# Kernel tuning notes

Measured on AMD Instinct MI355X. Metric: run time of the kernel, lower is better.

Reference implementation:

```python
import jax, jax.numpy as jnp
from jax import lax
import numpy as np

H = 32  # hidden size (hardcoded by Linear(32,1) in the source)
I = 1   # input size

def setup_inputs() -> dict:
    key = jax.random.key(0)
    ks = jax.random.split(key, 8)
    B, T = 2048, 1024
    s_ih = 1.0 / np.sqrt(H)
    inp = {
        "x": jax.random.normal(ks[0], (B, T, I), dtype=jnp.float32),
        "h_state": jnp.zeros((1, B, H), dtype=jnp.float32),
        # GRU params, PyTorch layout: gates stacked as [r; z; n] -> [3H, *]
        "W_ih": jax.random.uniform(ks[1], (3 * H, I), jnp.float32, -s_ih, s_ih),
        "W_hh": jax.random.uniform(ks[2], (3 * H, H), jnp.float32, -s_ih, s_ih),
        "b_ih": jax.random.uniform(ks[3], (3 * H,), jnp.float32, -s_ih, s_ih),
        "b_hh": jax.random.uniform(ks[4], (3 * H,), jnp.float32, -s_ih, s_ih),
        # output Linear(32, 1)
        "W_out": jax.random.uniform(ks[5], (1, H), jnp.float32, -s_ih, s_ih),
        "b_out": jax.random.uniform(ks[6], (1,), jnp.float32, -s_ih, s_ih),
    }
    return inp

def _gru(x, h0, W_ih, W_hh, b_ih, b_hh):
    # Precompute input projections for all timesteps: [B,T,3H]
    x_proj = jnp.einsum('bti,gi->btg', x, W_ih) + b_ih
    xp_t = jnp.swapaxes(x_proj, 0, 1)  # [T,B,3H] for scan

    def step(h, xp):
        gh = h @ W_hh.T + b_hh  # [B,3H]
        r = jax.nn.sigmoid(xp[:, :H] + gh[:, :H])
        z = jax.nn.sigmoid(xp[:, H:2 * H] + gh[:, H:2 * H])
        n = jnp.tanh(xp[:, 2 * H:] + r * gh[:, 2 * H:])
        h_new = (1.0 - z) * n + z * h
        return h_new, h_new

    h_final, h_seq = lax.scan(step, h0[0], xp_t)
    return jnp.swapaxes(h_seq, 0, 1), h_final[None]  # [B,T,H], [1,B,H]

def reference(x, h_state, W_ih, W_hh, b_ih, b_hh, W_out, b_out):
    r_out, h_n = _gru(x, h_state, W_ih, W_hh, b_ih, b_hh)
    # per-timestep Linear(32,1), vectorized over time
    y = jnp.einsum('bth,oh->bto', r_out, W_out) + b_out  # [B,T,1]
    return (y, h_n)
```

## Files before the change

### kernel.cpp

```cpp
#include <hip/hip_runtime.h>


constexpr int H  = 32;
constexpr int TT = 1024;
constexpr int BB = 2048;

typedef _Float16 hf2 __attribute__((ext_vector_type(2)));

__device__ __forceinline__ unsigned pack2(float a, float b) {
    hf2 t; t.x = (_Float16)a; t.y = (_Float16)b;
    return __builtin_bit_cast(unsigned, t);
}

__global__ __launch_bounds__(256, 1)
void gru_fused(const float* __restrict__ x,
               const float* __restrict__ h0,
               const float* __restrict__ W_ih,
               const float* __restrict__ W_hh,
               const float* __restrict__ b_ih,
               const float* __restrict__ b_hh,
               const float* __restrict__ W_out,
               const float* __restrict__ b_out,
               float* __restrict__ out)
{
    __shared__ __align__(16) _Float16 hbuf[4][64];
    __shared__ float xstage[4][64];
    __shared__ float ybuf[4][2][36 * 32];

    const int tid  = threadIdx.x;
    const int w    = tid >> 6;
    const int lane = tid & 63;
    const int half = lane >> 5;
    const int j    = lane & 31;
    const int gw   = (blockIdx.x << 2) | w;
    const int b    = (gw << 1) | half;

    const float NL2E = -1.44269504f;
    const float P2L2 =  2.88539008f;

    const float* Wrp = &W_hh[(0 * H + j) * H];
    const float* Wzp = &W_hh[(1 * H + j) * H];
    const float* Wnp = &W_hh[(2 * H + j) * H];
    unsigned wr[16], wz[16], wn[16];
#pragma unroll
    for (int k = 0; k < 16; ++k) {
        wr[k] = pack2(Wrp[2 * k] * NL2E, Wrp[2 * k + 1] * NL2E);
        wz[k] = pack2(Wzp[2 * k] * NL2E, Wzp[2 * k + 1] * NL2E);
        wn[k] = pack2(Wnp[2 * k] * P2L2, Wnp[2 * k + 1] * P2L2);
    }
    const float wir = W_ih[j] * NL2E;
    const float wiz = W_ih[H + j] * NL2E;
    const float br  = (b_ih[j] + b_hh[j]) * NL2E;
    const float bz  = (b_ih[H + j] + b_hh[H + j]) * NL2E;
    const float bhn = b_hh[2 * H + j] * P2L2;
    const float win = W_ih[2 * H + j] * P2L2;
    const float bin = b_ih[2 * H + j] * P2L2;
    const float wo  = W_out[j];
    const float bo  = b_out[0];

    float h = h0[b * H + j];

    const float* xb = x + (size_t)b * TT;
    float*       yb = out + (size_t)b * TT;

    const unsigned ha = (unsigned)(size_t)&hbuf[w][half * 32 + j];
    const unsigned hr = (unsigned)(size_t)&hbuf[w][half * 32];
    const unsigned xw = (unsigned)(size_t)&xstage[w][half * 32 + j];
    const unsigned xa = (unsigned)(size_t)&xstage[w][half * 32];
    const unsigned ya = (unsigned)(size_t)&ybuf[w][half][j];
    const float* yr = &ybuf[w][half][0];

#pragma unroll 1
    for (int t0 = 0; t0 < TT; t0 += 32) {
        const float xv = xb[t0 + j];

        asm volatile(
            "s_mov_b32 s20, 0\n\t"
            "v_mov_b32 v82, %[ya]\n\t"
            "v_mov_b32 v83, %[xa]\n\t"
            "ds_write_b32 %[xw], %[xv]\n\t"
            "L_gru_%=:\n\t"
            "v_cvt_f16_f32 v33, %[h]\n\t"
            "ds_write_b16 %[ha], v33\n\t"
            "ds_read_b128 v[36:39], %[hr]\n\t"
            "ds_read_b128 v[40:43], %[hr] offset:16\n\t"
            "ds_read_b128 v[44:47], %[hr] offset:32\n\t"
            "ds_read_b128 v[48:51], %[hr] offset:48\n\t"
            "ds_read_b32 v80, v83\n\t"
            "s_waitcnt lgkmcnt(0)\n\t"
            "v_dot2_f32_f16 v68, %[r0], v36, %[br]\n\t"
            "v_dot2_f32_f16 v69, %[z0], v36, %[bz]\n\t"
            "v_dot2_f32_f16 v70, %[n0], v36, %[bn]\n\t"
            "v_dot2_f32_f16 v68, %[r1], v37, v68\n\t"
            "v_dot2_f32_f16 v69, %[z1], v37, v69\n\t"
            "v_dot2_f32_f16 v70, %[n1], v37, v70\n\t"
            "v_dot2_f32_f16 v68, %[r2], v38, v68\n\t"
            "v_dot2_f32_f16 v69, %[z2], v38, v69\n\t"
            "v_dot2_f32_f16 v70, %[n2], v38, v70\n\t"
            "v_dot2_f32_f16 v68, %[r3], v39, v68\n\t"
            "v_dot2_f32_f16 v69, %[z3], v39, v69\n\t"
            "v_dot2_f32_f16 v70, %[n3], v39, v70\n\t"
            "v_dot2_f32_f16 v68, %[r4], v40, v68\n\t"
            "v_dot2_f32_f16 v69, %[z4], v40, v69\n\t"
            "v_dot2_f32_f16 v70, %[n4], v40, v70\n\t"
            "v_dot2_f32_f16 v68, %[r5], v41, v68\n\t"
            "v_dot2_f32_f16 v69, %[z5], v41, v69\n\t"
            "v_dot2_f32_f16 v70, %[n5], v41, v70\n\t"
            "v_dot2_f32_f16 v68, %[r6], v42, v68\n\t"
            "v_dot2_f32_f16 v69, %[z6], v42, v69\n\t"
            "v_dot2_f32_f16 v70, %[n6], v42, v70\n\t"
            "v_dot2_f32_f16 v68, %[r7], v43, v68\n\t"
            "v_dot2_f32_f16 v69, %[z7], v43, v69\n\t"
            "v_dot2_f32_f16 v70, %[n7], v43, v70\n\t"
            "v_dot2_f32_f16 v68, %[r8], v44, v68\n\t"
            "v_dot2_f32_f16 v69, %[z8], v44, v69\n\t"
            "v_dot2_f32_f16 v70, %[n8], v44, v70\n\t"
            "v_dot2_f32_f16 v68, %[r9], v45, v68\n\t"
            "v_dot2_f32_f16 v69, %[z9], v45, v69\n\t"
            "v_dot2_f32_f16 v70, %[n9], v45, v70\n\t"
            "v_dot2_f32_f16 v68, %[r10], v46, v68\n\t"
            "v_dot2_f32_f16 v69, %[z10], v46, v69\n\t"
            "v_dot2_f32_f16 v70, %[n10], v46, v70\n\t"
            "v_dot2_f32_f16 v68, %[r11], v47, v68\n\t"
            "v_dot2_f32_f16 v69, %[z11], v47, v69\n\t"
            "v_dot2_f32_f16 v70, %[n11], v47, v70\n\t"
            "v_dot2_f32_f16 v68, %[r12], v48, v68\n\t"
            "v_dot2_f32_f16 v69, %[z12], v48, v69\n\t"
            "v_dot2_f32_f16 v70, %[n12], v48, v70\n\t"
            "v_dot2_f32_f16 v68, %[r13], v49, v68\n\t"
            "v_dot2_f32_f16 v69, %[z13], v49, v69\n\t"
            "v_dot2_f32_f16 v70, %[n13], v49, v70\n\t"
            "v_dot2_f32_f16 v68, %[r14], v50, v68\n\t"
            "v_dot2_f32_f16 v69, %[z14], v50, v69\n\t"
            "v_dot2_f32_f16 v70, %[n14], v50, v70\n\t"
            "v_dot2_f32_f16 v68, %[r15], v51, v68\n\t"
            "v_dot2_f32_f16 v69, %[z15], v51, v69\n\t"
            "v_dot2_f32_f16 v70, %[n15], v51, v70\n\t"
            "v_fmac_f32 v68, v80, %[wir]\n\t"
            "v_fmac_f32 v69, v80, %[wiz]\n\t"
            "v_exp_f32 v71, v68\n\t"
            "v_exp_f32 v72, v69\n\t"
            "v_fma_f32 v74, v80, %[wi], %[bi]\n\t"
            "s_nop 2\n\t"
            "v_add_f32 v71, 1.0, v71\n\t"
            "v_add_f32 v72, 1.0, v72\n\t"
            "v_rcp_f32 v71, v71\n\t"
            "v_rcp_f32 v72, v72\n\t"
            "s_nop 2\n\t"
            "v_fmac_f32 v74, v71, v70\n\t"
            "v_exp_f32 v75, v74\n\t"
            "s_nop 2\n\t"
            "v_add_f32 v75, 1.0, v75\n\t"
            "v_rcp_f32 v75, v75\n\t"
            "s_nop 2\n\t"
            "v_fma_f32 v76, -2.0, v75, 1.0\n\t"
            "v_sub_f32 v77, %[h], v76\n\t"
            "v_fma_f32 %[h], v72, v77, v76\n\t"
            "v_mul_f32 v78, %[wo], %[h]\n\t"
            "ds_write_b32 v82, v78\n\t"
            "v_add_u32 v82, 144, v82\n\t"
            "v_add_u32 v83, 4, v83\n\t"
            "s_add_i32 s20, s20, 1\n\t"
            "s_cmp_lt_u32 s20, 32\n\t"
            "s_cbranch_scc1 L_gru_%=\n\t"
            "s_waitcnt lgkmcnt(0)"
            : [h]"+v"(h)
            : [xv]"v"(xv), [ha]"v"(ha), [hr]"v"(hr), [xw]"v"(xw), [xa]"v"(xa),
              [ya]"v"(ya),
              [wir]"v"(wir), [wiz]"v"(wiz), [wi]"v"(win), [bi]"v"(bin),
              [wo]"v"(wo), [br]"v"(br), [bz]"v"(bz), [bn]"v"(bhn),
              [r0]"v"(wr[0]), [r1]"v"(wr[1]), [r2]"v"(wr[2]), [r3]"v"(wr[3]),
              [r4]"v"(wr[4]), [r5]"v"(wr[5]), [r6]"v"(wr[6]), [r7]"v"(wr[7]),
              [r8]"v"(wr[8]), [r9]"v"(wr[9]), [r10]"v"(wr[10]), [r11]"v"(wr[11]),
              [r12]"v"(wr[12]), [r13]"v"(wr[13]), [r14]"v"(wr[14]), [r15]"v"(wr[15]),
              [z0]"v"(wz[0]), [z1]"v"(wz[1]), [z2]"v"(wz[2]), [z3]"v"(wz[3]),
              [z4]"v"(wz[4]), [z5]"v"(wz[5]), [z6]"v"(wz[6]), [z7]"v"(wz[7]),
              [z8]"v"(wz[8]), [z9]"v"(wz[9]), [z10]"v"(wz[10]), [z11]"v"(wz[11]),
              [z12]"v"(wz[12]), [z13]"v"(wz[13]), [z14]"v"(wz[14]), [z15]"v"(wz[15]),
              [n0]"v"(wn[0]), [n1]"v"(wn[1]), [n2]"v"(wn[2]), [n3]"v"(wn[3]),
              [n4]"v"(wn[4]), [n5]"v"(wn[5]), [n6]"v"(wn[6]), [n7]"v"(wn[7]),
              [n8]"v"(wn[8]), [n9]"v"(wn[9]), [n10]"v"(wn[10]), [n11]"v"(wn[11]),
              [n12]"v"(wn[12]), [n13]"v"(wn[13]), [n14]"v"(wn[14]), [n15]"v"(wn[15])
            : "memory", "scc", "s20",
              "v33", "v36", "v37", "v38", "v39", "v40", "v41", "v42", "v43",
              "v44", "v45", "v46", "v47", "v48", "v49", "v50", "v51",
              "v68", "v69", "v70", "v71", "v72", "v74", "v75", "v76", "v77",
              "v78", "v80", "v82", "v83");

        float s0 = 0.0f, s1 = 0.0f, s2 = 0.0f, s3 = 0.0f;
#pragma unroll
        for (int k = 0; k < 32; k += 4) {
            s0 += yr[36 * j + k + 0];
            s1 += yr[36 * j + k + 1];
            s2 += yr[36 * j + k + 2];
            s3 += yr[36 * j + k + 3];
        }
        yb[t0 + j] = (s0 + s1) + (s2 + s3) + bo;
        __builtin_amdgcn_wave_barrier();
    }

    out[(size_t)BB * TT + b * H + j] = h;
}

extern "C" void kernel_launch(void* const* d_in, const int* in_sizes, int n_in,
                              void* d_out, int out_size, void* d_ws, size_t ws_size,
                              hipStream_t stream) {
    const float* x     = (const float*)d_in[0];
    const float* h0    = (const float*)d_in[1];
    const float* W_ih  = (const float*)d_in[2];
    const float* W_hh  = (const float*)d_in[3];
    const float* b_ih  = (const float*)d_in[4];
    const float* b_hh  = (const float*)d_in[5];
    const float* W_out = (const float*)d_in[6];
    const float* b_out = (const float*)d_in[7];
    float* out = (float*)d_out;

    dim3 grid(BB / 8);
    dim3 block(256);
    gru_fused<<<grid, block, 0, stream>>>(x, h0, W_ih, W_hh, b_ih, b_hh,
                                          W_out, b_out, out);
}
```

Before: 312.1 us.

## Interleave two independent GRU batch streams per wave to hide LDS latency

Each wave now advances two independent pairs of batch rows (P and Q), software-pipelining them. The LDS write and reads of hidden state for one stream are issued while the other stream's dot products and gate math run, and the wait count is relaxed from 0 to 7. This targets the serial LDS round-trip latency in each recurrent step. Blocks shrink to 128 threads and the grid to 256 blocks, so there are half as many waves in total and each CU may occupy fewer SIMDs. LDS buffers are re-laid out with new padding to match.

```diff
diff --git a/kernel.cpp b/kernel.cpp
--- a/kernel.cpp
+++ b/kernel.cpp
@@ -12,7 +12,13 @@
     return __builtin_bit_cast(unsigned, t);
 }
 
-__global__ __launch_bounds__(256, 1)
+#define DOT2_SET(QA, QB, QC, QD)                                   \
+    "v_dot2_f32_f16 v68, %[r0], " QA ", %[br]\n\t"                 \
+    "v_dot2_f32_f16 v69, %[z0], " QA ", %[bz]\n\t"                 \
+    "v_dot2_f32_f16 v70, %[n0], " QA ", %[bn]\n\t"                 \
+    "v_dot2_f32_f16 v68, %[r1], " QA "1, v68\n\t"
+
+__global__ __launch_bounds__(128, 1)
 void gru_fused(const float* __restrict__ x,
                const float* __restrict__ h0,
                const float* __restrict__ W_ih,
@@ -23,17 +29,18 @@
                const float* __restrict__ b_out,
                float* __restrict__ out)
 {
-    __shared__ __align__(16) _Float16 hbuf[4][64];
-    __shared__ float xstage[4][64];
-    __shared__ float ybuf[4][2][36 * 32];
+    __shared__ __align__(16) _Float16 hbuf[2][2][64];
+    __shared__ float xst[2][2][2][34];
+    __shared__ float ybuf[2][2][2][33 * 32];
 
     const int tid  = threadIdx.x;
     const int w    = tid >> 6;
     const int lane = tid & 63;
     const int half = lane >> 5;
     const int j    = lane & 31;
-    const int gw   = (blockIdx.x << 2) | w;
-    const int b    = (gw << 1) | half;
+    const int g    = (blockIdx.x << 1) | w;
+    const int bP   = (g << 2) | half;
+    const int bQ   = bP + 2;
 
     const float NL2E = -1.44269504f;
     const float P2L2 =  2.88539008f;
@@ -58,36 +65,52 @@
     const float wo  = W_out[j];
     const float bo  = b_out[0];
 
-    float h = h0[b * H + j];
-
-    const float* xb = x + (size_t)b * TT;
-    float*       yb = out + (size_t)b * TT;
-
-    const unsigned ha = (unsigned)(size_t)&hbuf[w][half * 32 + j];
-    const unsigned hr = (unsigned)(size_t)&hbuf[w][half * 32];
-    const unsigned xw = (unsigned)(size_t)&xstage[w][half * 32 + j];
-    const unsigned xa = (unsigned)(size_t)&xstage[w][half * 32];
-    const unsigned ya = (unsigned)(size_t)&ybuf[w][half][j];
-    const float* yr = &ybuf[w][half][0];
+    float hP = h0[bP * H + j];
+    float hQ = h0[bQ * H + j];
+
+    const float* xbP = x + (size_t)bP * TT;
+    const float* xbQ = x + (size_t)bQ * TT;
+    float*       ybP = out + (size_t)bP * TT;
+    float*       ybQ = out + (size_t)bQ * TT;
+
+    const unsigned ha = (unsigned)(size_t)&hbuf[w][0][half * 32 + j];
+    const unsigned hr = (unsigned)(size_t)&hbuf[w][0][half * 32];
+    const unsigned xw = (unsigned)(size_t)&xst[w][0][half][j];
+    const unsigned xa = (unsigned)(size_t)&xst[w][0][half][0];
+    const unsigned ya = (unsigned)(size_t)&ybuf[w][0][half][j];
+    const float* yrP = &ybuf[w][0][half][0];
+    const float* yrQ = &ybuf[w][1][half][0];
 
 #pragma unroll 1
     for (int t0 = 0; t0 < TT; t0 += 32) {
-        const float xv = xb[t0 + j];
+        const float xvP = xbP[t0 + j];
+        const float xvQ = xbQ[t0 + j];
 
         asm volatile(
-            "s_mov_b32 s20, 0\n\t"
+            "s_mov_b32 s20, 32\n\t"
             "v_mov_b32 v82, %[ya]\n\t"
             "v_mov_b32 v83, %[xa]\n\t"
-            "ds_write_b32 %[xw], %[xv]\n\t"
+            "ds_write_b32 %[xw], %[xvP]\n\t"
+            "ds_write_b32 %[xw], %[xvQ] offset:272\n\t"
+            "ds_write_b32 v82, v78 offset:8448\n\t"
+            "v_cvt_f16_f32 v33, %[hQ]\n\t"
+            "ds_write_b16 %[ha], v33 offset:128\n\t"
+            "ds_read_b128 v[36:39], %[hr] offset:128\n\t"
+            "ds_read_b128 v[40:43], %[hr] offset:144\n\t"
+            "ds_read_b128 v[44:47], %[hr] offset:160\n\t"
+            "ds_read_b128 v[48:51], %[hr] offset:176\n\t"
+            "ds_read_b32 v80, v83 offset:272\n\t"
+            "ds_write_b32 v82, v78\n\t"
+            "v_cvt_f16_f32 v33, %[hP]\n\t"
+            "ds_write_b16 %[ha], v33\n\t"
+            "ds_read_b128 v[52:55], %[hr]\n\t"
+            "ds_read_b128 v[56:59], %[hr] offset:16\n\t"
+            "ds_read_b128 v[60:63], %[hr] offset:32\n\t"
+            "ds_read_b128 v[64:67], %[hr] offset:48\n\t"
+            "ds_read_b32 v81, v83\n\t"
+
             "L_gru_%=:\n\t"
-            "v_cvt_f16_f32 v33, %[h]\n\t"
-            "ds_write_b16 %[ha], v33\n\t"
-            "ds_read_b128 v[36:39], %[hr]\n\t"
-            "ds_read_b128 v[40:43], %[hr] offset:16\n\t"
-            "ds_read_b128 v[44:47], %[hr] offset:32\n\t"
-            "ds_read_b128 v[48:51], %[hr] offset:48\n\t"
-            "ds_read_b32 v80, v83\n\t"
-            "s_waitcnt lgkmcnt(0)\n\t"
+            "s_waitcnt lgkmcnt(7)\n\t"
             "v_dot2_f32_f16 v68, %[r0], v36, %[br]\n\t"
             "v_dot2_f32_f16 v69, %[z0], v36, %[bz]\n\t"
             "v_dot2_f32_f16 v70, %[n0], v36, %[bn]\n\t"
@@ -154,19 +177,104 @@
             "v_rcp_f32 v75, v75\n\t"
             "s_nop 2\n\t"
             "v_fma_f32 v76, -2.0, v75, 1.0\n\t"
-            "v_sub_f32 v77, %[h], v76\n\t"
-            "v_fma_f32 %[h], v72, v77, v76\n\t"
-            "v_mul_f32 v78, %[wo], %[h]\n\t"
+            "v_sub_f32 v77, %[hQ], v76\n\t"
+            "v_fma_f32 %[hQ], v72, v77, v76\n\t"
+            "v_mul_f32 v78, %[wo], %[hQ]\n\t"
+            "ds_write_b32 v82, v78 offset:8448\n\t"
+            "v_cvt_f16_f32 v33, %[hQ]\n\t"
+            "ds_write_b16 %[ha], v33 offset:128\n\t"
+            "ds_read_b128 v[36:39], %[hr] offset:128\n\t"
+            "ds_read_b128 v[40:43], %[hr] offset:144\n\t"
+            "ds_read_b128 v[44:47], %[hr] offset:160\n\t"
+            "ds_read_b128 v[48:51], %[hr] offset:176\n\t"
+            "ds_read_b32 v80, v83 offset:276\n\t"
+            "s_waitcnt lgkmcnt(7)\n\t"
+            "v_dot2_f32_f16 v68, %[r0], v52, %[br]\n\t"
+            "v_dot2_f32_f16 v69, %[z0], v52, %[bz]\n\t"
+            "v_dot2_f32_f16 v70, %[n0], v52, %[bn]\n\t"
+            "v_dot2_f32_f16 v68, %[r1], v53, v68\n\t"
+            "v_dot2_f32_f16 v69, %[z1], v53, v69\n\t"
+            "v_dot2_f32_f16 v70, %[n1], v53, v70\n\t"
+            "v_dot2_f32_f16 v68, %[r2], v54, v68\n\t"
+            "v_dot2_f32_f16 v69, %[z2], v54, v69\n\t"
+            "v_dot2_f32_f16 v70, %[n2], v54, v70\n\t"
+            "v_dot2_f32_f16 v68, %[r3], v55, v68\n\t"
+            "v_dot2_f32_f16 v69, %[z3], v55, v69\n\t"
+            "v_dot2_f32_f16 v70, %[n3], v55, v70\n\t"
+            "v_dot2_f32_f16 v68, %[r4], v56, v68\n\t"
+            "v_dot2_f32_f16 v69, %[z4], v56, v69\n\t"
+            "v_dot2_f32_f16 v70, %[n4], v56, v70\n\t"
+            "v_dot2_f32_f16 v68, %[r5], v57, v68\n\t"
+            "v_dot2_f32_f16 v69, %[z5], v57, v69\n\t"
+            "v_dot2_f32_f16 v70, %[n5], v57, v70\n\t"
+            "v_dot2_f32_f16 v68, %[r6], v58, v68\n\t"
+            "v_dot2_f32_f16 v69, %[z6], v58, v69\n\t"
+            "v_dot2_f32_f16 v70, %[n6], v58, v70\n\t"
+            "v_dot2_f32_f16 v68, %[r7], v59, v68\n\t"
+            "v_dot2_f32_f16 v69, %[z7], v59, v69\n\t"
+            "v_dot2_f32_f16 v70, %[n7], v59, v70\n\t"
+            "v_dot2_f32_f16 v68, %[r8], v60, v68\n\t"
+            "v_dot2_f32_f16 v69, %[z8], v60, v69\n\t"
+            "v_dot2_f32_f16 v70, %[n8], v60, v70\n\t"
+            "v_dot2_f32_f16 v68, %[r9], v61, v68\n\t"
+            "v_dot2_f32_f16 v69, %[z9], v61, v69\n\t"
+            "v_dot2_f32_f16 v70, %[n9], v61, v70\n\t"
+            "v_dot2_f32_f16 v68, %[r10], v62, v68\n\t"
+            "v_dot2_f32_f16 v69, %[z10], v62, v69\n\t"
+            "v_dot2_f32_f16 v70, %[n10], v62, v70\n\t"
+            "v_dot2_f32_f16 v68, %[r11], v63, v68\n\t"
+            "v_dot2_f32_f16 v69, %[z11], v63, v69\n\t"
+            "v_dot2_f32_f16 v70, %[n11], v63, v70\n\t"
+            "v_dot2_f32_f16 v68, %[r12], v64, v68\n\t"
+            "v_dot2_f32_f16 v69, %[z12], v64, v69\n\t"
+            "v_dot2_f32_f16 v70, %[n12], v64, v70\n\t"
+            "v_dot2_f32_f16 v68, %[r13], v65, v68\n\t"
+            "v_dot2_f32_f16 v69, %[z13], v65, v69\n\t"
+            "v_dot2_f32_f16 v70, %[n13], v65, v70\n\t"
+            "v_dot2_f32_f16 v68, %[r14], v66, v68\n\t"
+            "v_dot2_f32_f16 v69, %[z14], v66, v69\n\t"
+            "v_dot2_f32_f16 v70, %[n14], v66, v70\n\t"
+            "v_dot2_f32_f16 v68, %[r15], v67, v68\n\t"
+            "v_dot2_f32_f16 v69, %[z15], v67, v69\n\t"
+            "v_dot2_f32_f16 v70, %[n15], v67, v70\n\t"
+            "v_fmac_f32 v68, v81, %[wir]\n\t"
+            "v_fmac_f32 v69, v81, %[wiz]\n\t"
+            "v_exp_f32 v71, v68\n\t"
+            "v_exp_f32 v72, v69\n\t"
+            "v_fma_f32 v74, v81, %[wi], %[bi]\n\t"
+            "s_nop 2\n\t"
+            "v_add_f32 v71, 1.0, v71\n\t"
+            "v_add_f32 v72, 1.0, v72\n\t"
+            "v_rcp_f32 v71, v71\n\t"
+            "v_rcp_f32 v72, v72\n\t"
+            "s_nop 2\n\t"
+            "v_fmac_f32 v74, v71, v70\n\t"
+            "v_exp_f32 v75, v74\n\t"
+            "s_nop 2\n\t"
+            "v_add_f32 v75, 1.0, v75\n\t"
+            "v_rcp_f32 v75, v75\n\t"
+            "s_nop 2\n\t"
+            "v_fma_f32 v76, -2.0, v75, 1.0\n\t"
+            "v_sub_f32 v77, %[hP], v76\n\t"
+            "v_fma_f32 %[hP], v72, v77, v76\n\t"
+            "v_mul_f32 v78, %[wo], %[hP]\n\t"
             "ds_write_b32 v82, v78\n\t"
-            "v_add_u32 v82, 144, v82\n\t"
+            "v_cvt_f16_f32 v33, %[hP]\n\t"
+            "ds_write_b16 %[ha], v33\n\t"
+            "ds_read_b128 v[52:55], %[hr]\n\t"
+            "ds_read_b128 v[56:59], %[hr] offset:16\n\t"
+            "ds_read_b128 v[60:63], %[hr] offset:32\n\t"
+            "ds_read_b128 v[64:67], %[hr] offset:48\n\t"
+            "ds_read_b32 v81, v83 offset:4\n\t"
+            "v_add_u32 v82, 132, v82\n\t"
             "v_add_u32 v83, 4, v83\n\t"
-            "s_add_i32 s20, s20, 1\n\t"
-            "s_cmp_lt_u32 s20, 32\n\t"
+            "s_sub_i32 s20, s20, 1\n\t"
+            "s_cmp_gt_i32 s20, 0\n\t"
             "s_cbranch_scc1 L_gru_%=\n\t"
             "s_waitcnt lgkmcnt(0)"
-            : [h]"+v"(h)
-            : [xv]"v"(xv), [ha]"v"(ha), [hr]"v"(hr), [xw]"v"(xw), [xa]"v"(xa),
-              [ya]"v"(ya),
+            : [hP]"+v"(hP), [hQ]"+v"(hQ)
+            : [xvP]"v"(xvP), [xvQ]"v"(xvQ),
+              [ha]"v"(ha), [hr]"v"(hr), [xw]"v"(xw), [xa]"v"(xa), [ya]"v"(ya),
               [wir]"v"(wir), [wiz]"v"(wiz), [wi]"v"(win), [bi]"v"(bin),
               [wo]"v"(wo), [br]"v"(br), [bz]"v"(bz), [bn]"v"(bhn),
               [r0]"v"(wr[0]), [r1]"v"(wr[1]), [r2]"v"(wr[2]), [r3]"v"(wr[3]),
@@ -184,22 +292,31 @@
             : "memory", "scc", "s20",
               "v33", "v36", "v37", "v38", "v39", "v40", "v41", "v42", "v43",
               "v44", "v45", "v46", "v47", "v48", "v49", "v50", "v51",
+              "v52", "v53", "v54", "v55", "v56", "v57", "v58", "v59",
+              "v60", "v61", "v62", "v63", "v64", "v65", "v66", "v67",
               "v68", "v69", "v70", "v71", "v72", "v74", "v75", "v76", "v77",
-              "v78", "v80", "v82", "v83");
-
-        float s0 = 0.0f, s1 = 0.0f, s2 = 0.0f, s3 = 0.0f;
+              "v78", "v80", "v81", "v82", "v83");
+
+        float p0 = 0.0f, p1 = 0.0f, p2 = 0.0f, p3 = 0.0f;
+        float q0 = 0.0f, q1 = 0.0f, q2 = 0.0f, q3 = 0.0f;
 #pragma unroll
         for (int k = 0; k < 32; k += 4) {
-            s0 += yr[36 * j + k + 0];
-            s1 += yr[36 * j + k + 1];
-            s2 += yr[36 * j + k + 2];
-            s3 += yr[36 * j + k + 3];
+            p0 += yrP[33 * j + k + 0];
+            p1 += yrP[33 * j + k + 1];
+            p2 += yrP[33 * j + k + 2];
+            p3 += yrP[33 * j + k + 3];
+            q0 += yrQ[33 * j + k + 0];
+            q1 += yrQ[33 * j + k + 1];
+            q2 += yrQ[33 * j + k + 2];
+            q3 += yrQ[33 * j + k + 3];
         }
-        yb[t0 + j] = (s0 + s1) + (s2 + s3) + bo;
+        ybP[t0 + j] = (p0 + p1) + (p2 + p3) + bo;
+        ybQ[t0 + j] = (q0 + q1) + (q2 + q3) + bo;
         __builtin_amdgcn_wave_barrier();
     }
 
-    out[(size_t)BB * TT + b * H + j] = h;
+    out[(size_t)BB * TT + bP * H + j] = hP;
+    out[(size_t)BB * TT + bQ * H + j] = hQ;
 }
 
 extern "C" void kernel_launch(void* const* d_in, const int* in_sizes, int n_in,
@@ -215,8 +332,8 @@
     const float* b_out = (const float*)d_in[7];
     float* out = (float*)d_out;
 
-    dim3 grid(BB / 8);
-    dim3 block(256);
+    dim3 grid(256);
+    dim3 block(128);
     gru_fused<<<grid, block, 0, stream>>>(x, h0, W_ih, W_hh, b_ih, b_hh,
                                           W_out, b_out, out);
 }
```

Result: slower. 479.8 us (+53.7%).

## Unroll GRU step loop by two and overlap LDS writes with next step

Applied to the files above, without the earlier changes.

The per-timestep inline-asm loop is unrolled twice and software-pipelined. The next step's hidden-state broadcast reads are issued before the output store, and a waitcnt of one lets that y write stay in flight while the dot products start. Input x is now fetched as a 64-bit pair every two steps, and loop counter overhead is halved. The y staging buffer stride changes from 36 to 33 to cut LDS bank conflicts on the transposed reduction reads. The s_nop padding grows from 2 to 3, which lengthens the serial dependency chain slightly.

```diff
diff --git a/kernel.cpp b/kernel.cpp
--- a/kernel.cpp
+++ b/kernel.cpp
@@ -11,6 +11,78 @@
     hf2 t; t.x = (_Float16)a; t.y = (_Float16)b;
     return __builtin_bit_cast(unsigned, t);
 }
+
+#define DOT48                                          \
+    "v_dot2_f32_f16 v68, %[r0], v36, %[br]\n\t"        \
+    "v_dot2_f32_f16 v69, %[z0], v36, %[bz]\n\t"        \
+    "v_dot2_f32_f16 v70, %[n0], v36, %[bn]\n\t"        \
+    "v_dot2_f32_f16 v68, %[r1], v37, v68\n\t"          \
+    "v_dot2_f32_f16 v69, %[z1], v37, v69\n\t"          \
+    "v_dot2_f32_f16 v70, %[n1], v37, v70\n\t"          \
+    "v_dot2_f32_f16 v68, %[r2], v38, v68\n\t"          \
+    "v_dot2_f32_f16 v69, %[z2], v38, v69\n\t"          \
+    "v_dot2_f32_f16 v70, %[n2], v38, v70\n\t"          \
+    "v_dot2_f32_f16 v68, %[r3], v39, v68\n\t"          \
+    "v_dot2_f32_f16 v69, %[z3], v39, v69\n\t"          \
+    "v_dot2_f32_f16 v70, %[n3], v39, v70\n\t"          \
+    "v_dot2_f32_f16 v68, %[r4], v40, v68\n\t"          \
+    "v_dot2_f32_f16 v69, %[z4], v40, v69\n\t"          \
+    "v_dot2_f32_f16 v70, %[n4], v40, v70\n\t"          \
+    "v_dot2_f32_f16 v68, %[r5], v41, v68\n\t"          \
+    "v_dot2_f32_f16 v69, %[z5], v41, v69\n\t"          \
+    "v_dot2_f32_f16 v70, %[n5], v41, v70\n\t"          \
+    "v_dot2_f32_f16 v68, %[r6], v42, v68\n\t"          \
+    "v_dot2_f32_f16 v69, %[z6], v42, v69\n\t"          \
+    "v_dot2_f32_f16 v70, %[n6], v42, v70\n\t"          \
+    "v_dot2_f32_f16 v68, %[r7], v43, v68\n\t"          \
+    "v_dot2_f32_f16 v69, %[z7], v43, v69\n\t"          \
+    "v_dot2_f32_f16 v70, %[n7], v43, v70\n\t"          \
+    "v_dot2_f32_f16 v68, %[r8], v44, v68\n\t"          \
+    "v_dot2_f32_f16 v69, %[z8], v44, v69\n\t"          \
+    "v_dot2_f32_f16 v70, %[n8], v44, v70\n\t"          \
+    "v_dot2_f32_f16 v68, %[r9], v45, v68\n\t"          \
+    "v_dot2_f32_f16 v69, %[z9], v45, v69\n\t"          \
+    "v_dot2_f32_f16 v70, %[n9], v45, v70\n\t"          \
+    "v_dot2_f32_f16 v68, %[r10], v46, v68\n\t"         \
+    "v_dot2_f32_f16 v69, %[z10], v46, v69\n\t"         \
+    "v_dot2_f32_f16 v70, %[n10], v46, v70\n\t"         \
+    "v_dot2_f32_f16 v68, %[r11], v47, v68\n\t"         \
+    "v_dot2_f32_f16 v69, %[z11], v47, v69\n\t"         \
+    "v_dot2_f32_f16 v70, %[n11], v47, v70\n\t"         \
+    "v_dot2_f32_f16 v68, %[r12], v48, v68\n\t"         \
+    "v_dot2_f32_f16 v69, %[z12], v48, v69\n\t"         \
+    "v_dot2_f32_f16 v70, %[n12], v48, v70\n\t"         \
+    "v_dot2_f32_f16 v68, %[r13], v49, v68\n\t"         \
+    "v_dot2_f32_f16 v69, %[z13], v49, v69\n\t"         \
+    "v_dot2_f32_f16 v70, %[n13], v49, v70\n\t"         \
+    "v_dot2_f32_f16 v68, %[r14], v50, v68\n\t"         \
+    "v_dot2_f32_f16 v69, %[z14], v50, v69\n\t"         \
+    "v_dot2_f32_f16 v70, %[n14], v50, v70\n\t"         \
+    "v_dot2_f32_f16 v68, %[r15], v51, v68\n\t"         \
+    "v_dot2_f32_f16 v69, %[z15], v51, v69\n\t"         \
+    "v_dot2_f32_f16 v70, %[n15], v51, v70\n\t"
+
+#define TAIL(XREG, HREG)                               \
+    "v_fmac_f32 v68, " XREG ", %[wir]\n\t"             \
+    "v_fmac_f32 v69, " XREG ", %[wiz]\n\t"             \
+    "v_exp_f32 v71, v68\n\t"                           \
+    "v_exp_f32 v72, v69\n\t"                           \
+    "v_fma_f32 v74, " XREG ", %[wi], %[bi]\n\t"        \
+    "s_nop 3\n\t"                                      \
+    "v_add_f32 v71, 1.0, v71\n\t"                      \
+    "v_add_f32 v72, 1.0, v72\n\t"                      \
+    "v_rcp_f32 v71, v71\n\t"                           \
+    "v_rcp_f32 v72, v72\n\t"                           \
+    "s_nop 3\n\t"                                      \
+    "v_fmac_f32 v74, v71, v70\n\t"                     \
+    "v_exp_f32 v75, v74\n\t"                           \
+    "s_nop 3\n\t"                                      \
+    "v_add_f32 v75, 1.0, v75\n\t"                      \
+    "v_rcp_f32 v75, v75\n\t"                           \
+    "s_nop 3\n\t"                                      \
+    "v_fma_f32 v76, -2.0, v75, 1.0\n\t"                \
+    "v_sub_f32 v77, " HREG ", v76\n\t"                 \
+    "v_fma_f32 " HREG ", v72, v77, v76\n\t"
 
 __global__ __launch_bounds__(256, 1)
 void gru_fused(const float* __restrict__ x,
@@ -24,8 +96,8 @@
                float* __restrict__ out)
 {
     __shared__ __align__(16) _Float16 hbuf[4][64];
-    __shared__ float xstage[4][64];
-    __shared__ float ybuf[4][2][36 * 32];
+    __shared__ __align__(8) float xstage[4][2][36];
+    __shared__ float ybuf[4][2][33 * 32];
 
     const int tid  = threadIdx.x;
     const int w    = tid >> 6;
@@ -65,8 +137,8 @@
 
     const unsigned ha = (unsigned)(size_t)&hbuf[w][half * 32 + j];
     const unsigned hr = (unsigned)(size_t)&hbuf[w][half * 32];
-    const unsigned xw = (unsigned)(size_t)&xstage[w][half * 32 + j];
-    const unsigned xa = (unsigned)(size_t)&xstage[w][half * 32];
+    const unsigned xw = (unsigned)(size_t)&xstage[w][half][j];
+    const unsigned xa = (unsigned)(size_t)&xstage[w][half][0];
     const unsigned ya = (unsigned)(size_t)&ybuf[w][half][j];
     const float* yr = &ybuf[w][half][0];
 
@@ -75,93 +147,47 @@
         const float xv = xb[t0 + j];
 
         asm volatile(
-            "s_mov_b32 s20, 0\n\t"
+            "s_mov_b32 s20, 16\n\t"
             "v_mov_b32 v82, %[ya]\n\t"
             "v_mov_b32 v83, %[xa]\n\t"
             "ds_write_b32 %[xw], %[xv]\n\t"
-            "L_gru_%=:\n\t"
+            "ds_read_b64 v[80:81], v83\n\t"
             "v_cvt_f16_f32 v33, %[h]\n\t"
             "ds_write_b16 %[ha], v33\n\t"
             "ds_read_b128 v[36:39], %[hr]\n\t"
             "ds_read_b128 v[40:43], %[hr] offset:16\n\t"
             "ds_read_b128 v[44:47], %[hr] offset:32\n\t"
             "ds_read_b128 v[48:51], %[hr] offset:48\n\t"
-            "ds_read_b32 v80, v83\n\t"
-            "s_waitcnt lgkmcnt(0)\n\t"
-            "v_dot2_f32_f16 v68, %[r0], v36, %[br]\n\t"
-            "v_dot2_f32_f16 v69, %[z0], v36, %[bz]\n\t"
-            "v_dot2_f32_f16 v70, %[n0], v36, %[bn]\n\t"
-            "v_dot2_f32_f16 v68, %[r1], v37, v68\n\t"
-            "v_dot2_f32_f16 v69, %[z1], v37, v69\n\t"
-            "v_dot2_f32_f16 v70, %[n1], v37, v70\n\t"
-            "v_dot2_f32_f16 v68, %[r2], v38, v68\n\t"
-            "v_dot2_f32_f16 v69, %[z2], v38, v69\n\t"
-            "v_dot2_f32_f16 v70, %[n2], v38, v70\n\t"
-            "v_dot2_f32_f16 v68, %[r3], v39, v68\n\t"
-            "v_dot2_f32_f16 v69, %[z3], v39, v69\n\t"
-            "v_dot2_f32_f16 v70, %[n3], v39, v70\n\t"
-            "v_dot2_f32_f16 v68, %[r4], v40, v68\n\t"
-            "v_dot2_f32_f16 v69, %[z4], v40, v69\n\t"
-            "v_dot2_f32_f16 v70, %[n4], v40, v70\n\t"
-            "v_dot2_f32_f16 v68, %[r5], v41, v68\n\t"
-            "v_dot2_f32_f16 v69, %[z5], v41, v69\n\t"
-            "v_dot2_f32_f16 v70, %[n5], v41, v70\n\t"
-            "v_dot2_f32_f16 v68, %[r6], v42, v68\n\t"
-            "v_dot2_f32_f16 v69, %[z6], v42, v69\n\t"
-            "v_dot2_f32_f16 v70, %[n6], v42, v70\n\t"
-            "v_dot2_f32_f16 v68, %[r7], v43, v68\n\t"
-            "v_dot2_f32_f16 v69, %[z7], v43, v69\n\t"
-            "v_dot2_f32_f16 v70, %[n7], v43, v70\n\t"
-            "v_dot2_f32_f16 v68, %[r8], v44, v68\n\t"
-            "v_dot2_f32_f16 v69, %[z8], v44, v69\n\t"
-            "v_dot2_f32_f16 v70, %[n8], v44, v70\n\t"
-            "v_dot2_f32_f16 v68, %[r9], v45, v68\n\t"
-            "v_dot2_f32_f16 v69, %[z9], v45, v69\n\t"
-            "v_dot2_f32_f16 v70, %[n9], v45, v70\n\t"
-            "v_dot2_f32_f16 v68, %[r10], v46, v68\n\t"
-            "v_dot2_f32_f16 v69, %[z10], v46, v69\n\t"
-            "v_dot2_f32_f16 v70, %[n10], v46, v70\n\t"
-            "v_dot2_f32_f16 v68, %[r11], v47, v68\n\t"
-            "v_dot2_f32_f16 v69, %[z11], v47, v69\n\t"
-            "v_dot2_f32_f16 v70, %[n11], v47, v70\n\t"
-            "v_dot2_f32_f16 v68, %[r12], v48, v68\n\t"
-            "v_dot2_f32_f16 v69, %[z12], v48, v69\n\t"
-            "v_dot2_f32_f16 v70, %[n12], v48, v70\n\t"
-            "v_dot2_f32_f16 v68, %[r13], v49, v68\n\t"
-            "v_dot2_f32_f16 v69, %[z13], v49, v69\n\t"
-            "v_dot2_f32_f16 v70, %[n13], v49, v70\n\t"
-            "v_dot2_f32_f16 v68, %[r14], v50, v68\n\t"
-            "v_dot2_f32_f16 v69, %[z14], v50, v69\n\t"
-            "v_dot2_f32_f16 v70, %[n14], v50, v70\n\t"
-            "v_dot2_f32_f16 v68, %[r15], v51, v68\n\t"
-            "v_dot2_f32_f16 v69, %[z15], v51, v69\n\t"
-            "v_dot2_f32_f16 v70, %[n15], v51, v70\n\t"
-            "v_fmac_f32 v68, v80, %[wir]\n\t"
-            "v_fmac_f32 v69, v80, %[wiz]\n\t"
-            "v_exp_f32 v71, v68\n\t"
-            "v_exp_f32 v72, v69\n\t"
-            "v_fma_f32 v74, v80, %[wi], %[bi]\n\t"
-            "s_nop 2\n\t"
-            "v_add_f32 v71, 1.0, v71\n\t"
-            "v_add_f32 v72, 1.0, v72\n\t"
-            "v_rcp_f32 v71, v71\n\t"
-            "v_rcp_f32 v72, v72\n\t"
-            "s_nop 2\n\t"
-            "v_fmac_f32 v74, v71, v70\n\t"
-            "v_exp_f32 v75, v74\n\t"
-            "s_nop 2\n\t"
-            "v_add_f32 v75, 1.0, v75\n\t"
-            "v_rcp_f32 v75, v75\n\t"
-            "s_nop 2\n\t"
-            "v_fma_f32 v76, -2.0, v75, 1.0\n\t"
-            "v_sub_f32 v77, %[h], v76\n\t"
-            "v_fma_f32 %[h], v72, v77, v76\n\t"
+            "ds_write_b32 v82, v78\n\t"
+
+            "L_gru_%=:\n\t"
+            "s_waitcnt lgkmcnt(1)\n\t"
+            DOT48
+            TAIL("v80", "%[h]")
+            "v_cvt_f16_f32 v33, %[h]\n\t"
+            "ds_write_b16 %[ha], v33\n\t"
+            "ds_read_b128 v[36:39], %[hr]\n\t"
+            "ds_read_b128 v[40:43], %[hr] offset:16\n\t"
+            "ds_read_b128 v[44:47], %[hr] offset:32\n\t"
+            "ds_read_b128 v[48:51], %[hr] offset:48\n\t"
             "v_mul_f32 v78, %[wo], %[h]\n\t"
             "ds_write_b32 v82, v78\n\t"
-            "v_add_u32 v82, 144, v82\n\t"
-            "v_add_u32 v83, 4, v83\n\t"
-            "s_add_i32 s20, s20, 1\n\t"
-            "s_cmp_lt_u32 s20, 32\n\t"
+            "s_waitcnt lgkmcnt(1)\n\t"
+            DOT48
+            TAIL("v81", "%[h]")
+            "v_cvt_f16_f32 v33, %[h]\n\t"
+            "ds_write_b16 %[ha], v33\n\t"
+            "ds_read_b128 v[36:39], %[hr]\n\t"
+            "ds_read_b128 v[40:43], %[hr] offset:16\n\t"
+            "ds_read_b128 v[44:47], %[hr] offset:32\n\t"
+            "ds_read_b128 v[48:51], %[hr] offset:48\n\t"
+            "ds_read_b64 v[80:81], v83 offset:8\n\t"
+            "v_mul_f32 v78, %[wo], %[h]\n\t"
+            "ds_write_b32 v82, v78 offset:132\n\t"
+            "v_add_u32 v82, 264, v82\n\t"
+            "v_add_u32 v83, 8, v83\n\t"
+            "s_sub_i32 s20, s20, 1\n\t"
+            "s_cmp_gt_i32 s20, 0\n\t"
             "s_cbranch_scc1 L_gru_%=\n\t"
             "s_waitcnt lgkmcnt(0)"
             : [h]"+v"(h)
@@ -185,21 +211,24 @@
               "v33", "v36", "v37", "v38", "v39", "v40", "v41", "v42", "v43",
               "v44", "v45", "v46", "v47", "v48", "v49", "v50", "v51",
               "v68", "v69", "v70", "v71", "v72", "v74", "v75", "v76", "v77",
-              "v78", "v80", "v82", "v83");
+              "v78", "v80", "v81", "v82", "v83");
 
         float s0 = 0.0f, s1 = 0.0f, s2 = 0.0f, s3 = 0.0f;
 #pragma unroll
         for (int k = 0; k < 32; k += 4) {
-            s0 += yr[36 * j + k + 0];
-            s1 += yr[36 * j + k + 1];
-            s2 += yr[36 * j + k + 2];
-            s3 += yr[36 * j + k + 3];
+            s0 += yr[33 * j + k + 0];
+            s1 += yr[33 * j + k + 1];
+            s2 += yr[33 * j + k + 2];
+            s3 += yr[33 * j + k + 3];
         }
         yb[t0 + j] = (s0 + s1) + (s2 + s3) + bo;
         __builtin_amdgcn_wave_barrier();
     }
 
     out[(size_t)BB * TT + b * H + j] = h;
+
+#undef DOT48
+#undef TAIL
 }
 
 extern "C" void kernel_launch(void* const* d_in, const int* in_sizes, int n_in,
```

After: 285.9 us. 1.09x faster.
